# Kernel tuning notes

Measured on AMD Instinct MI355X. Metric: run time of the kernel, lower is better.

## Reference

```python
import jax, jax.numpy as jnp
import numpy as np

N = 100000   # nodes
E = 1600000  # edges
IN = 32      # in_channels
ED = 16      # edge_dim
G = 128      # num graphs in batch
NEG = 0.01   # LeakyReLU default slope

def lrelu(v):
    return jnp.where(v > 0, v, NEG * v)

def gine_conv(x, src, dst, edge_attr, We, be, Wa, ba, Wb, bb):
    # PyG GINEConv (eps=0): out = nn(x + sum_{j->i} relu(x_j + lin(edge_attr)))
    e = edge_attr @ We + be                      # [E, d]
    m = jax.nn.relu(x[src] + e)                  # gather + add + relu
    agg = jax.ops.segment_sum(m, dst, num_segments=x.shape[0])
    h = x + agg
    return lrelu(h @ Wa + ba) @ Wb + bb

def setup_inputs() -> dict:
    key = jax.random.key(0)
    ks = jax.random.split(key, 24)
    w = lambda k, shape: (jax.random.normal(k, shape, dtype=jnp.float32) * 0.05)
    inp = {
        "x": jax.random.normal(ks[0], (N, IN), dtype=jnp.float32),
        "edge_index": jax.random.randint(ks[1], (2, E), 0, N),
        "edge_attr": jax.random.normal(ks[2], (E, ED), dtype=jnp.float32),
        "batch": jnp.sort(jax.random.randint(ks[3], (N,), 0, G)),
        # conv1: edge lin ED->IN, nn IN->32->64
        "We1": w(ks[4], (ED, IN)), "be1": w(ks[5], (IN,)),
        "W1a": w(ks[6], (IN, 32)), "b1a": w(ks[7], (32,)),
        "W1b": w(ks[8], (32, 64)), "b1b": w(ks[9], (64,)),
        # conv2: edge lin ED->64, nn 64->128->256
        "We2": w(ks[10], (ED, 64)), "be2": w(ks[11], (64,)),
        "W2a": w(ks[12], (64, 128)), "b2a": w(ks[13], (128,)),
        "W2b": w(ks[14], (128, 256)), "b2b": w(ks[15], (256,)),
        # head
        "Wf0": w(ks[16], (256, 128)), "bf0": w(ks[17], (128,)),
        "Wf1": w(ks[18], (128, 64)), "bf1": w(ks[19], (64,)),
        "Wf2": w(ks[20], (64, 32)), "bf2": w(ks[21], (32,)),
        "Wr": w(ks[22], (32, 1)), "br": w(ks[23], (1,)),
    }
    return inp

def reference(x, edge_index, edge_attr, batch,
              We1, be1, W1a, b1a, W1b, b1b,
              We2, be2, W2a, b2a, W2b, b2b,
              Wf0, bf0, Wf1, bf1, Wf2, bf2, Wr, br):
    src, dst = edge_index[0], edge_index[1]
    h = gine_conv(x, src, dst, edge_attr, We1, be1, W1a, b1a, W1b, b1b)
    h = lrelu(h)
    h = gine_conv(h, src, dst, edge_attr, We2, be2, W2a, b2a, W2b, b2b)
    h = lrelu(h)
    # global_add_pool over graph ids
    g = jax.ops.segment_sum(h, batch, num_segments=G)   # [G, 256]
    g = lrelu(g @ Wf0 + bf0)
    # dropout: identity (inference reference)
    g = lrelu(g @ Wf1 + bf1)
    g = lrelu(g @ Wf2 + bf2)
    out = (g @ Wr + br)[:, 0]                           # squeeze(dim=1)
    return out
```

## Files before the change

### kernel.cpp

```cpp
#include <hip/hip_runtime.h>

__device__ __forceinline__ float lrelu(float v){ return v > 0.f ? v : 0.01f*v; }

typedef __attribute__((ext_vector_type(8))) short v8s;
typedef __attribute__((ext_vector_type(4))) float v4f;

__device__ __forceinline__ unsigned short f2bf(float f){
    union{float f; unsigned int i;} v; v.f = f;
    unsigned int u = v.i;
    return (unsigned short)((u + 0x7fffu + ((u >> 16) & 1u)) >> 16);
}
__device__ __forceinline__ unsigned int pack2(float a, float b){
    return (unsigned int)f2bf(a) | ((unsigned int)f2bf(b) << 16);
}
__device__ __forceinline__ float bflo(unsigned int u){
    union{unsigned int i; float f;} v; v.i = u << 16; return v.f;
}
__device__ __forceinline__ float bfhi(unsigned int u){
    union{unsigned int i; float f;} v; v.i = u & 0xffff0000u; return v.f;
}
__device__ __forceinline__ float bf2f(unsigned short s){
    union{unsigned int i; float f;} v; v.i = ((unsigned int)s) << 16; return v.f;
}

__global__ __launch_bounds__(256) void k_hist(
    const int* __restrict__ ei, int* __restrict__ deg, int E)
{
    int e = blockIdx.x * 256 + threadIdx.x;
    if (e >= E) return;
    atomicAdd(&deg[ei[E + e]], 1);
}

__global__ __launch_bounds__(256) void k_scan1(
    const int* __restrict__ deg, int* __restrict__ rowptr,
    int* __restrict__ bsum, int N)
{
    __shared__ int sh[256];
    int t = threadIdx.x;
    int i = blockIdx.x * 256 + t;
    int v = (i < N) ? deg[i] : 0;
    sh[t] = v;
    __syncthreads();
    #pragma unroll
    for (int off = 1; off < 256; off <<= 1) {
        int add = (t >= off) ? sh[t - off] : 0;
        __syncthreads();
        sh[t] += add;
        __syncthreads();
    }
    if (i < N) rowptr[i] = sh[t] - v;
    if (t == 255) bsum[blockIdx.x] = sh[t];
}

__global__ __launch_bounds__(512) void k_scan2(int* __restrict__ bsum, int nb)
{
    __shared__ int sh[512];
    int t = threadIdx.x;
    int v = (t < nb) ? bsum[t] : 0;
    sh[t] = v;
    __syncthreads();
    #pragma unroll
    for (int off = 1; off < 512; off <<= 1) {
        int add = (t >= off) ? sh[t - off] : 0;
        __syncthreads();
        sh[t] += add;
        __syncthreads();
    }
    if (t < nb) bsum[t] = sh[t] - v;
}

__global__ __launch_bounds__(256) void k_scan3(
    int* __restrict__ rowptr, int* __restrict__ cursor,
    const int* __restrict__ bsum, int N)
{
    int i = blockIdx.x * 256 + threadIdx.x;
    if (i >= N) return;
    int rp = rowptr[i] + bsum[i >> 8];
    rowptr[i] = rp;
    cursor[i] = rp;
}

__global__ __launch_bounds__(256) void k_castx(
    const float* __restrict__ x, unsigned int* __restrict__ xb, int M8)
{
    int i = blockIdx.x * 256 + threadIdx.x;
    if (i >= M8) return;
    const float4* p = reinterpret_cast<const float4*>(x) + (size_t)i * 2;
    float4 a = p[0], b = p[1];
    uint4 o;
    o.x = pack2(a.x, a.y); o.y = pack2(a.z, a.w);
    o.z = pack2(b.x, b.y); o.w = pack2(b.z, b.w);
    reinterpret_cast<uint4*>(xb)[i] = o;
}

__global__ __launch_bounds__(256) void k_castw(
    const float* __restrict__ W2a, const float* __restrict__ W2b,
    const float* __restrict__ We1, const float* __restrict__ We2,
    unsigned short* __restrict__ W2aT, unsigned short* __restrict__ W2bT,
    unsigned short* __restrict__ WeT1, unsigned short* __restrict__ WeT2)
{
    int i = blockIdx.x * 256 + threadIdx.x;
    if (i < 128 * 64) {
        int n = i >> 6, k = i & 63;
        W2aT[i] = f2bf(W2a[k * 128 + n]);
    }
    int j = i - 128 * 64;
    if (j >= 0 && j < 256 * 128) {
        int n = j >> 7, k = j & 127;
        W2bT[j] = f2bf(W2b[k * 256 + n]);
    }
    int q1 = i - (128 * 64 + 256 * 128);
    if (q1 >= 0 && q1 < 32 * 32) {
        int cch = q1 >> 5, k = q1 & 31;
        WeT1[q1] = (k < 16) ? f2bf(We1[k * 32 + cch]) : (unsigned short)0;
    }
    int q2 = q1 - 32 * 32;
    if (q2 >= 0 && q2 < 64 * 32) {
        int cch = q2 >> 5, k = q2 & 31;
        WeT2[q2] = (k < 16) ? f2bf(We2[k * 64 + cch]) : (unsigned short)0;
    }
}

#define RCHUNK 2048
__global__ __launch_bounds__(256) void k_scatter(
    const int* __restrict__ ei, const float* __restrict__ ea,
    int* __restrict__ cursor, int2* __restrict__ csr2,
    uint4* __restrict__ eab, int E, int N)
{
    const int r = blockIdx.x & 7;
    const int c = blockIdx.x >> 3;
    const int rspan = (N + 7) >> 3;
    const int lo = r * rspan;
    const int hi = lo + rspan;
    int base = c * RCHUNK;
    int end = base + RCHUNK; if (end > E) end = E;
    for (int e = base + threadIdx.x; e < end; e += 256) {
        int d = ei[E + e];
        if (d >= lo && d < hi) {
            int s = ei[e];
            int slot = atomicAdd(&cursor[d], 1);
            const float4* p = reinterpret_cast<const float4*>(ea) + (size_t)e * 4;
            float4 a = p[0], b = p[1], cc = p[2], f = p[3];
            uint4 o0, o1;
            o0.x = pack2(a.x, a.y);  o0.y = pack2(a.z, a.w);
            o0.z = pack2(b.x, b.y);  o0.w = pack2(b.z, b.w);
            o1.x = pack2(cc.x, cc.y); o1.y = pack2(cc.z, cc.w);
            o1.z = pack2(f.x, f.y);  o1.w = pack2(f.z, f.w);
            eab[(size_t)slot * 2]     = o0;
            eab[(size_t)slot * 2 + 1] = o1;
            int2 rr; rr.x = s; rr.y = d;
            csr2[slot] = rr;
        }
    }
}

#define AGG_SPW 64

__global__ __launch_bounds__(256) void k_agg2(
    const unsigned short* __restrict__ xb,
    const uint4* __restrict__ eab,
    const unsigned short* __restrict__ WeT,
    const float* __restrict__ be,
    const int2* __restrict__ csr2, float* __restrict__ agg, int E)
{
    __shared__ __align__(16) float lds[4][2][16][68];
    const int tid  = threadIdx.x;
    const int wv   = tid >> 6;
    const int lane = tid & 63;
    const int lid  = lane & 15;
    const int quad = lane >> 4;
    const int wave = __builtin_amdgcn_readfirstlane((blockIdx.x * 256 + tid) >> 6);
    const int s0 = wave * AGG_SPW;
    if (s0 >= E) return;
    const int nsl = (s0 + AGG_SPW <= E) ? AGG_SPW : E - s0;

    v8s af0 = *reinterpret_cast<const v8s*>(WeT + lid * 32 + quad * 8);
    v8s af1 = *reinterpret_cast<const v8s*>(WeT + (16 + lid) * 32 + quad * 8);
    v8s af2 = *reinterpret_cast<const v8s*>(WeT + (32 + lid) * 32 + quad * 8);
    v8s af3 = *reinterpret_cast<const v8s*>(WeT + (48 + lid) * 32 + quad * 8);
    const float biasc = be[lane];
    const int2*  cp = csr2 + s0;
    const uint4* ep = eab + (size_t)s0 * 2;

    unsigned short xv[2][16];
    int dsv[2][16];
    float acc = 0.f;
    int   cur = cp[0].y;
    bool  owned = false;

    auto GATHER = [&](int t) {
        const int base = t * 16;
        const int cnt = nsl - base;
        #pragma unroll
        for (int e = 0; e < 16; ++e) {
            int ee = (e < cnt) ? e : cnt - 1;
            int2 r = cp[base + ee];
            dsv[t & 1][e] = r.y;
            xv[t & 1][e] = xb[(unsigned)r.x * 64u + (unsigned)lane];
        }
    };
    auto MFMA = [&](int t) {
        int sl = t * 16 + lid;
        if (sl > nsl - 1) sl = nsl - 1;
        uint4 bw = {0u, 0u, 0u, 0u};
        if (quad < 2) bw = ep[2 * sl + quad];
        union { uint4 u; v8s s; } uu; uu.u = bw;
        v8s bf = uu.s;
        v4f d0 = {0.f, 0.f, 0.f, 0.f}, d1 = d0, d2 = d0, d3 = d0;
        d0 = __builtin_amdgcn_mfma_f32_16x16x32_bf16(af0, bf, d0, 0, 0, 0);
        d1 = __builtin_amdgcn_mfma_f32_16x16x32_bf16(af1, bf, d1, 0, 0, 0);
        d2 = __builtin_amdgcn_mfma_f32_16x16x32_bf16(af2, bf, d2, 0, 0, 0);
        d3 = __builtin_amdgcn_mfma_f32_16x16x32_bf16(af3, bf, d3, 0, 0, 0);
        float* lp = &lds[wv][t & 1][lid][quad * 4];
        *reinterpret_cast<v4f*>(lp)      = d0;
        *reinterpret_cast<v4f*>(lp + 16) = d1;
        *reinterpret_cast<v4f*>(lp + 32) = d2;
        *reinterpret_cast<v4f*>(lp + 48) = d3;
    };
    auto ACCUM = [&](int t) {
        const int cnt = nsl - t * 16;
        #pragma unroll
        for (int e = 0; e < 16; ++e) {
            if (e < cnt) {
                float ls = lds[wv][t & 1][e][lane];
                float m = ls + biasc + bf2f(xv[t & 1][e]);
                m = m > 0.f ? m : 0.f;
                int d = dsv[t & 1][e];
                if (d != cur) {
                    if (owned) agg[(unsigned)cur * 64u + lane] = acc;
                    else       atomicAdd(&agg[(unsigned)cur * 64u + lane], acc);
                    acc = 0.f; cur = d; owned = true;
                }
                acc += m;
            }
        }
    };

    GATHER(0); MFMA(0);
    #pragma unroll
    for (int t = 0; t < 4; ++t) {
        if (t * 16 < nsl) {
            if ((t + 1) < 4 && (t + 1) * 16 < nsl) { GATHER(t + 1); MFMA(t + 1); }
            ACCUM(t);
        }
    }
    atomicAdd(&agg[(unsigned)cur * 64u + lane], acc);
}

__global__ __launch_bounds__(256) void k_agg1(
    const unsigned short* __restrict__ xb,
    const uint4* __restrict__ eab,
    const unsigned short* __restrict__ WeT,
    const float* __restrict__ be,
    const int2* __restrict__ csr2, float* __restrict__ agg, int E)
{
    __shared__ __align__(16) float lds[4][2][16][36];
    const int tid  = threadIdx.x;
    const int wv   = tid >> 6;
    const int lane = tid & 63;
    const int lid  = lane & 15;
    const int quad = lane >> 4;
    const int c    = lane & 31;
    const int sub  = lane >> 5;
    const int wave = __builtin_amdgcn_readfirstlane((blockIdx.x * 256 + tid) >> 6);
    const int s0 = wave * AGG_SPW;
    if (s0 >= E) return;
    const int nsl = (s0 + AGG_SPW <= E) ? AGG_SPW : E - s0;

    v8s af0 = *reinterpret_cast<const v8s*>(WeT + lid * 32 + quad * 8);
    v8s af1 = *reinterpret_cast<const v8s*>(WeT + (16 + lid) * 32 + quad * 8);
    const float biasc = be[c];
    const int2*  cp = csr2 + s0;
    const uint4* ep = eab + (size_t)s0 * 2;

    unsigned short xv[2][8];
    int dsv[2][8];
    float acc = 0.f;
    int cur = cp[(sub < nsl) ? sub : 0].y;

    auto GATHER = [&](int t) {
        #pragma unroll
        for (int i = 0; i < 8; ++i) {
            int e = t * 16 + 2 * i + sub;
            int ee = (e < nsl) ? e : nsl - 1;
            int2 r = cp[ee];
            dsv[t & 1][i] = r.y;
            xv[t & 1][i] = xb[(unsigned)r.x * 32u + (unsigned)c];
        }
    };
    auto MFMA = [&](int t) {
        int sl = t * 16 + lid;
        if (sl > nsl - 1) sl = nsl - 1;
        uint4 bw = {0u, 0u, 0u, 0u};
        if (quad < 2) bw = ep[2 * sl + quad];
        union { uint4 u; v8s s; } uu; uu.u = bw;
        v8s bf = uu.s;
        v4f d0 = {0.f, 0.f, 0.f, 0.f}, d1 = d0;
        d0 = __builtin_amdgcn_mfma_f32_16x16x32_bf16(af0, bf, d0, 0, 0, 0);
        d1 = __builtin_amdgcn_mfma_f32_16x16x32_bf16(af1, bf, d1, 0, 0, 0);
        float* lp = &lds[wv][t & 1][lid][quad * 4];
        *reinterpret_cast<v4f*>(lp)      = d0;
        *reinterpret_cast<v4f*>(lp + 16) = d1;
    };
    auto ACCUM = [&](int t) {
        #pragma unroll
        for (int i = 0; i < 8; ++i) {
            int e = t * 16 + 2 * i + sub;
            if (e < nsl) {
                float ls = lds[wv][t & 1][2 * i + sub][c];
                float m = ls + biasc + bf2f(xv[t & 1][i]);
                m = m > 0.f ? m : 0.f;
                int d = dsv[t & 1][i];
                if (d != cur) {
                    atomicAdd(&agg[(unsigned)cur * 32u + c], acc);
                    acc = 0.f; cur = d;
                }
                acc += m;
            }
        }
    };

    GATHER(0); MFMA(0);
    #pragma unroll
    for (int t = 0; t < 4; ++t) {
        if (t * 16 < nsl) {
            if ((t + 1) < 4 && (t + 1) * 16 < nsl) { GATHER(t + 1); MFMA(t + 1); }
            ACCUM(t);
        }
    }
    atomicAdd(&agg[(unsigned)cur * 32u + c], acc);
}

__global__ __launch_bounds__(256, 4) void k_mlp1(
    const float* __restrict__ x, const float* __restrict__ agg1,
    const float* __restrict__ W1a, const float* __restrict__ b1a,
    const float* __restrict__ W1b, const float* __restrict__ b1b,
    unsigned int* __restrict__ h1b, int N)
{
    __shared__ float ts[64][33];
    const int tid = threadIdx.x;
    const int n0 = blockIdx.x * 64;
    const int row = tid & 63;
    const int grp = __builtin_amdgcn_readfirstlane(tid >> 6);
    const int g = n0 + row;

    float hv[32];
    if (g < N) {
        const float4* xp = reinterpret_cast<const float4*>(x) + (size_t)g * 8;
        const float4* ap = reinterpret_cast<const float4*>(agg1) + (size_t)g * 8;
        #pragma unroll
        for (int q = 0; q < 8; ++q) {
            float4 a = xp[q], b = ap[q];
            hv[4*q+0]=a.x+b.x; hv[4*q+1]=a.y+b.y;
            hv[4*q+2]=a.z+b.z; hv[4*q+3]=a.w+b.w;
        }
    } else {
        #pragma unroll
        for (int q = 0; q < 32; ++q) hv[q] = 0.f;
    }

    {
        const int c0 = grp * 8;
        float acc[8];
        #pragma unroll
        for (int i = 0; i < 8; ++i) acc[i] = b1a[c0 + i];
        for (int k = 0; k < 32; ++k) {
            float h = hv[k];
            const float* w = W1a + k*32 + c0;
            #pragma unroll
            for (int i = 0; i < 8; ++i) acc[i] = fmaf(h, w[i], acc[i]);
        }
        #pragma unroll
        for (int i = 0; i < 8; ++i) ts[row][c0 + i] = lrelu(acc[i]);
    }
    __syncthreads();

    {
        const int c0 = grp * 16;
        float acc[16];
        #pragma unroll
        for (int i = 0; i < 16; ++i) acc[i] = b1b[c0 + i];
        for (int k = 0; k < 32; ++k) {
            float tv = ts[row][k];
            const float* w = W1b + k*64 + c0;
            #pragma unroll
            for (int i = 0; i < 16; ++i) acc[i] = fmaf(tv, w[i], acc[i]);
        }
        if (g < N) {
            #pragma unroll
            for (int i = 0; i < 16; ++i) acc[i] = lrelu(acc[i]);
            uint4 p0, p1;
            p0.x = pack2(acc[0],  acc[1]);  p0.y = pack2(acc[2],  acc[3]);
            p0.z = pack2(acc[4],  acc[5]);  p0.w = pack2(acc[6],  acc[7]);
            p1.x = pack2(acc[8],  acc[9]);  p1.y = pack2(acc[10], acc[11]);
            p1.z = pack2(acc[12], acc[13]); p1.w = pack2(acc[14], acc[15]);
            uint4* bp = reinterpret_cast<uint4*>(h1b + (size_t)g*32 + (c0>>1));
            bp[0] = p0; bp[1] = p1;
        }
    }
}

__global__ __launch_bounds__(256) void k_mlp2(
    const unsigned int* __restrict__ h1b, const float* __restrict__ agg2,
    const unsigned short* __restrict__ W2aT, const float* __restrict__ b2a,
    const unsigned short* __restrict__ W2bT, const float* __restrict__ b2b,
    unsigned short* __restrict__ h2b, int N)
{
    __shared__ unsigned short hs[64][72];
    __shared__ unsigned short ts[64][136];
    const int tid = threadIdx.x;
    const int n0 = blockIdx.x * 64;

    {
        int r = tid >> 2, cseg = (tid & 3) * 16;
        int g = n0 + r;
        uint4 o0 = {0,0,0,0}, o1 = {0,0,0,0};
        if (g < N) {
            const uint4* hp = reinterpret_cast<const uint4*>(
                                  h1b + (size_t)g*32 + (cseg>>1));
            const float4* ap = reinterpret_cast<const float4*>(agg2)
                               + (size_t)g*16 + (cseg>>2);
            uint4 u0 = hp[0], u1 = hp[1];
            float4 b0=ap[0], b1=ap[1], b2=ap[2], b3=ap[3];
            o0.x = pack2(bflo(u0.x)+b0.x, bfhi(u0.x)+b0.y);
            o0.y = pack2(bflo(u0.y)+b0.z, bfhi(u0.y)+b0.w);
            o0.z = pack2(bflo(u0.z)+b1.x, bfhi(u0.z)+b1.y);
            o0.w = pack2(bflo(u0.w)+b1.z, bfhi(u0.w)+b1.w);
            o1.x = pack2(bflo(u1.x)+b2.x, bfhi(u1.x)+b2.y);
            o1.y = pack2(bflo(u1.y)+b2.z, bfhi(u1.y)+b2.w);
            o1.z = pack2(bflo(u1.z)+b3.x, bfhi(u1.z)+b3.y);
            o1.w = pack2(bflo(u1.w)+b3.z, bfhi(u1.w)+b3.w);
        }
        uint4* dp = reinterpret_cast<uint4*>(&hs[r][cseg]);
        dp[0] = o0; dp[1] = o1;
    }
    __syncthreads();

    const int wv   = __builtin_amdgcn_readfirstlane(tid >> 6);
    const int lane = tid & 63;
    const int lid  = lane & 15;
    const int quad = lane >> 4;

    v8s afA0 = *reinterpret_cast<const v8s*>(&hs[wv*16 + lid][quad*8]);
    v8s afA1 = *reinterpret_cast<const v8s*>(&hs[wv*16 + lid][32 + quad*8]);
    #pragma unroll
    for (int nt = 0; nt < 8; ++nt) {
        v4f acc = {0.f, 0.f, 0.f, 0.f};
        const unsigned short* wp = W2aT + (nt*16 + lid)*64 + quad*8;
        v8s b0 = *reinterpret_cast<const v8s*>(wp);
        v8s b1 = *reinterpret_cast<const v8s*>(wp + 32);
        acc = __builtin_amdgcn_mfma_f32_16x16x32_bf16(afA0, b0, acc, 0, 0, 0);
        acc = __builtin_amdgcn_mfma_f32_16x16x32_bf16(afA1, b1, acc, 0, 0, 0);
        float bias = b2a[nt*16 + lid];
        #pragma unroll
        for (int i = 0; i < 4; ++i) {
            float v = lrelu(acc[i] + bias);
            ts[wv*16 + quad*4 + i][nt*16 + lid] = f2bf(v);
        }
    }
    __syncthreads();

    v8s afB[4];
    #pragma unroll
    for (int ks = 0; ks < 4; ++ks)
        afB[ks] = *reinterpret_cast<const v8s*>(&ts[wv*16 + lid][ks*32 + quad*8]);
    const int gbase = n0 + wv*16 + quad*4;
    #pragma unroll 4
    for (int nt = 0; nt < 16; ++nt) {
        v4f acc = {0.f, 0.f, 0.f, 0.f};
        const unsigned short* wp = W2bT + (nt*16 + lid)*128 + quad*8;
        #pragma unroll
        for (int ks = 0; ks < 4; ++ks) {
            v8s bf = *reinterpret_cast<const v8s*>(wp + ks*32);
            acc = __builtin_amdgcn_mfma_f32_16x16x32_bf16(afB[ks], bf, acc, 0, 0, 0);
        }
        float bias = b2b[nt*16 + lid];
        #pragma unroll
        for (int i = 0; i < 4; ++i) {
            int g = gbase + i;
            if (g < N) {
                float v = lrelu(acc[i] + bias);
                h2b[(size_t)g*256 + nt*16 + lid] = f2bf(v);
            }
        }
    }
}

__global__ __launch_bounds__(256) void k_pool(
    const unsigned int* __restrict__ h2b, const int* __restrict__ batch,
    float* __restrict__ g, int N)
{
    int tid = threadIdx.x;
    int c2 = tid & 127;
    int h = tid >> 7;
    int base = blockIdx.x * 128;
    int n0 = base + h;
    int nend = base + 128; if (nend > N) nend = N;
    if (n0 >= N) return;
    float acc0 = 0.f, acc1 = 0.f;
    int cur = batch[n0];
    for (int n = n0; n < nend; n += 2) {
        int b = batch[n];
        unsigned int hv = h2b[(size_t)n * 128 + c2];
        if (b != cur) {
            atomicAdd(&g[(unsigned)cur * 256 + 2*c2],     acc0);
            atomicAdd(&g[(unsigned)cur * 256 + 2*c2 + 1], acc1);
            acc0 = acc1 = 0.f; cur = b;
        }
        acc0 += bflo(hv); acc1 += bfhi(hv);
    }
    atomicAdd(&g[(unsigned)cur * 256 + 2*c2],     acc0);
    atomicAdd(&g[(unsigned)cur * 256 + 2*c2 + 1], acc1);
}

__global__ __launch_bounds__(256) void k_head(
    const float* __restrict__ g,
    const float* __restrict__ Wf0, const float* __restrict__ bf0,
    const float* __restrict__ Wf1, const float* __restrict__ bf1,
    const float* __restrict__ Wf2, const float* __restrict__ bf2,
    const float* __restrict__ Wr,  const float* __restrict__ br,
    float* __restrict__ out)
{
    __shared__ float buf[256];
    __shared__ float t0[128];
    __shared__ float t1[64];
    __shared__ float t2[32];
    int gid = blockIdx.x, tid = threadIdx.x;
    buf[tid] = g[(size_t)gid*256 + tid];
    __syncthreads();
    if (tid < 128) {
        float acc = bf0[tid];
        for (int k = 0; k < 256; ++k) acc = fmaf(buf[k], Wf0[k*128 + tid], acc);
        t0[tid] = lrelu(acc);
    }
    __syncthreads();
    if (tid < 64) {
        float acc = bf1[tid];
        for (int k = 0; k < 128; ++k) acc = fmaf(t0[k], Wf1[k*64 + tid], acc);
        t1[tid] = lrelu(acc);
    }
    __syncthreads();
    if (tid < 32) {
        float acc = bf2[tid];
        for (int k = 0; k < 64; ++k) acc = fmaf(t1[k], Wf2[k*32 + tid], acc);
        t2[tid] = lrelu(acc);
    }
    __syncthreads();
    if (tid == 0) {
        float acc = br[0];
        for (int k = 0; k < 32; ++k) acc = fmaf(t2[k], Wr[k], acc);
        out[gid] = acc;
    }
}

extern "C" void kernel_launch(void* const* d_in, const int* in_sizes, int n_in,
                              void* d_out, int out_size, void* d_ws, size_t ws_size,
                              hipStream_t stream)
{
    const float* x     = (const float*)d_in[0];
    const int*   ei    = (const int*)d_in[1];
    const float* ea    = (const float*)d_in[2];
    const int*   batch = (const int*)d_in[3];
    const float* We1=(const float*)d_in[4],  *be1=(const float*)d_in[5];
    const float* W1a=(const float*)d_in[6],  *b1a=(const float*)d_in[7];
    const float* W1b=(const float*)d_in[8],  *b1b=(const float*)d_in[9];
    const float* We2=(const float*)d_in[10], *be2=(const float*)d_in[11];
    const float* W2a=(const float*)d_in[12], *b2a=(const float*)d_in[13];
    const float* W2b=(const float*)d_in[14], *b2b=(const float*)d_in[15];
    const float* Wf0=(const float*)d_in[16], *bf0=(const float*)d_in[17];
    const float* Wf1=(const float*)d_in[18], *bf1=(const float*)d_in[19];
    const float* Wf2=(const float*)d_in[20], *bf2=(const float*)d_in[21];
    const float* Wr =(const float*)d_in[22], *br =(const float*)d_in[23];

    const int N = in_sizes[0] / 32;
    const int E = in_sizes[1] / 2;
    const int G = out_size;
    const int nb = (N + 255) / 256;
    const int nb64 = (N + 63) / 64;

    char* p = (char*)d_ws;
    int*   deg     = (int*)p;                 p += (size_t)N * 4;
    float* gbuf    = (float*)p;               p += (size_t)G * 256 * 4;
    float* agg1    = (float*)p;               p += (size_t)N * 32 * 4;
    float* agg2    = (float*)p;               p += (size_t)N * 64 * 4;
    size_t zero_bytes = (size_t)(p - (char*)d_ws);
    int*   rowptr  = (int*)p;                 p += (size_t)N * 4;
    int*   cursor  = (int*)p;                 p += (size_t)N * 4;
    int*   bsum    = (int*)p;                 p += 512 * 4;
    p = (char*)(((uintptr_t)p + 63) & ~(uintptr_t)63);
    int2*  csr2    = (int2*)p;                p += (size_t)E * 8;
    uint4* eab     = (uint4*)p;               p += (size_t)E * 32;
    unsigned short* xb   = (unsigned short*)p; p += (size_t)N * 32 * 2;
    unsigned int*   h1b  = (unsigned int*)p;  p += (size_t)N * 64 * 2;
    unsigned short* W2aT = (unsigned short*)p; p += 128 * 64 * 2;
    unsigned short* W2bT = (unsigned short*)p; p += 256 * 128 * 2;
    unsigned short* WeT1 = (unsigned short*)p; p += 32 * 32 * 2;
    unsigned short* WeT2 = (unsigned short*)p; p += 64 * 32 * 2;
    unsigned short* h2b  = (unsigned short*)p; p += (size_t)N * 256 * 2;

    hipMemsetAsync(d_ws, 0, zero_bytes, stream);

    int eb = (E + 255) / 256;

    k_hist   <<<eb, 256, 0, stream>>>(ei, deg, E);
    k_scan1  <<<nb, 256, 0, stream>>>(deg, rowptr, bsum, N);
    k_scan2  <<<1, 512, 0, stream>>>(bsum, nb);
    k_scan3  <<<nb, 256, 0, stream>>>(rowptr, cursor, bsum, N);
    {
        int M8 = N * 32 / 8;
        k_castx<<<(M8 + 255) / 256, 256, 0, stream>>>(x, (unsigned int*)xb, M8);
    }
    {
        int tot = 128*64 + 256*128 + 32*32 + 64*32;
        k_castw<<<(tot + 255) / 256, 256, 0, stream>>>(W2a, W2b, We1, We2,
                                                       W2aT, W2bT, WeT1, WeT2);
    }
    {
        int nchunks = (E + RCHUNK - 1) / RCHUNK;
        k_scatter<<<nchunks * 8, 256, 0, stream>>>(ei, ea, cursor, csr2, eab,
                                                   E, N);
    }

    {
        int waves = (E + AGG_SPW - 1) / AGG_SPW;
        int blocks = (waves + 3) / 4;
        k_agg1<<<blocks, 256, 0, stream>>>(xb, eab, WeT1, be1, csr2, agg1, E);
    }
    k_mlp1<<<nb64, 256, 0, stream>>>(x, agg1, W1a, b1a, W1b, b1b,
                                     (unsigned int*)h1b, N);

    {
        int waves = (E + AGG_SPW - 1) / AGG_SPW;
        int blocks = (waves + 3) / 4;
        k_agg2<<<blocks, 256, 0, stream>>>((const unsigned short*)h1b, eab, WeT2,
                                           be2, csr2, agg2, E);
    }
    k_mlp2<<<nb64, 256, 0, stream>>>(h1b, agg2, W2aT, b2a, W2bT, b2b, h2b, N);

    k_pool<<<(N + 127) / 128, 256, 0, stream>>>((const unsigned int*)h2b, batch,
                                                gbuf, N);
    k_head<<<G, 256, 0, stream>>>(gbuf, Wf0, bf0, Wf1, bf1, Wf2, bf2, Wr, br,
                                  (float*)d_out);
}
```

Baseline: 678.7 us.

## Replace CSR scatter with two-pass bucketed radix-style edge ordering

```diff
diff --git a/kernel.cpp b/kernel.cpp
--- a/kernel.cpp
+++ b/kernel.cpp
@@ -78,6 +78,14 @@
     int rp = rowptr[i] + bsum[i >> 8];
     rowptr[i] = rp;
     cursor[i] = rp;
+}
+
+__global__ __launch_bounds__(512) void k_binit(
+    const int* __restrict__ rowptr, int* __restrict__ bcur, int N)
+{
+    int b = threadIdx.x;
+    int node = b << 8;
+    if (node < N) bcur[b] = rowptr[node];
 }
 
 __global__ __launch_bounds__(256) void k_castx(
@@ -121,36 +129,63 @@
     }
 }
 
-#define RCHUNK 2048
-__global__ __launch_bounds__(256) void k_scatter(
+#define BCH 4096
+__global__ __launch_bounds__(256) void k_bucket(
     const int* __restrict__ ei, const float* __restrict__ ea,
-    int* __restrict__ cursor, int2* __restrict__ csr2,
-    uint4* __restrict__ eab, int E, int N)
-{
-    const int r = blockIdx.x & 7;
-    const int c = blockIdx.x >> 3;
-    const int rspan = (N + 7) >> 3;
-    const int lo = r * rspan;
-    const int hi = lo + rspan;
-    int base = c * RCHUNK;
-    int end = base + RCHUNK; if (end > E) end = E;
-    for (int e = base + threadIdx.x; e < end; e += 256) {
+    int* __restrict__ bcur, int2* __restrict__ sA, uint4* __restrict__ sB,
+    int E)
+{
+    __shared__ int hist[512];
+    __shared__ int base[512];
+    __shared__ int lcur[512];
+    const int tid = threadIdx.x;
+    const int c0 = blockIdx.x * BCH;
+    int cend = c0 + BCH; if (cend > E) cend = E;
+    hist[tid] = 0; hist[tid + 256] = 0;
+    __syncthreads();
+    for (int e = c0 + tid; e < cend; e += 256)
+        atomicAdd(&hist[ei[E + e] >> 8], 1);
+    __syncthreads();
+    {
+        int h0 = hist[tid], h1 = hist[tid + 256];
+        base[tid]       = h0 ? atomicAdd(&bcur[tid], h0) : 0;
+        base[tid + 256] = h1 ? atomicAdd(&bcur[tid + 256], h1) : 0;
+        lcur[tid] = 0; lcur[tid + 256] = 0;
+    }
+    __syncthreads();
+    for (int e = c0 + tid; e < cend; e += 256) {
         int d = ei[E + e];
-        if (d >= lo && d < hi) {
-            int s = ei[e];
-            int slot = atomicAdd(&cursor[d], 1);
-            const float4* p = reinterpret_cast<const float4*>(ea) + (size_t)e * 4;
-            float4 a = p[0], b = p[1], cc = p[2], f = p[3];
-            uint4 o0, o1;
-            o0.x = pack2(a.x, a.y);  o0.y = pack2(a.z, a.w);
-            o0.z = pack2(b.x, b.y);  o0.w = pack2(b.z, b.w);
-            o1.x = pack2(cc.x, cc.y); o1.y = pack2(cc.z, cc.w);
-            o1.z = pack2(f.x, f.y);  o1.w = pack2(f.z, f.w);
-            eab[(size_t)slot * 2]     = o0;
-            eab[(size_t)slot * 2 + 1] = o1;
-            int2 rr; rr.x = s; rr.y = d;
-            csr2[slot] = rr;
-        }
+        int b = d >> 8;
+        int pos = base[b] + atomicAdd(&lcur[b], 1);
+        int s = ei[e];
+        const float4* p = reinterpret_cast<const float4*>(ea) + (size_t)e * 4;
+        float4 a = p[0], bb = p[1], cc = p[2], f = p[3];
+        uint4 o0, o1;
+        o0.x = pack2(a.x, a.y);   o0.y = pack2(a.z, a.w);
+        o0.z = pack2(bb.x, bb.y); o0.w = pack2(bb.z, bb.w);
+        o1.x = pack2(cc.x, cc.y); o1.y = pack2(cc.z, cc.w);
+        o1.z = pack2(f.x, f.y);   o1.w = pack2(f.z, f.w);
+        sB[(size_t)pos * 2]     = o0;
+        sB[(size_t)pos * 2 + 1] = o1;
+        int2 rr; rr.x = s; rr.y = d;
+        sA[pos] = rr;
+    }
+}
+
+__global__ __launch_bounds__(256) void k_order(
+    const int2* __restrict__ sA, const uint4* __restrict__ sB,
+    const int* __restrict__ rowptr, int* __restrict__ cursor,
+    int2* __restrict__ csr2, uint4* __restrict__ eab, int E, int NBK)
+{
+    int b = blockIdx.x;
+    int s0 = rowptr[b << 8];
+    int e0 = (b + 1 < NBK) ? rowptr[(b + 1) << 8] : E;
+    for (int i = s0 + threadIdx.x; i < e0; i += 256) {
+        int2 r = sA[i];
+        int slot = atomicAdd(&cursor[r.y], 1);
+        csr2[slot] = r;
+        eab[(size_t)slot * 2]     = sB[(size_t)i * 2];
+        eab[(size_t)slot * 2 + 1] = sB[(size_t)i * 2 + 1];
     }
 }
 
@@ -577,6 +612,7 @@
     const int G = out_size;
     const int nb = (N + 255) / 256;
     const int nb64 = (N + 63) / 64;
+    const int NBK = (N + 255) >> 8;
 
     char* p = (char*)d_ws;
     int*   deg     = (int*)p;                 p += (size_t)N * 4;
@@ -587,9 +623,11 @@
     int*   rowptr  = (int*)p;                 p += (size_t)N * 4;
     int*   cursor  = (int*)p;                 p += (size_t)N * 4;
     int*   bsum    = (int*)p;                 p += 512 * 4;
+    int*   bcur    = (int*)p;                 p += 512 * 4;
     p = (char*)(((uintptr_t)p + 63) & ~(uintptr_t)63);
     int2*  csr2    = (int2*)p;                p += (size_t)E * 8;
     uint4* eab     = (uint4*)p;               p += (size_t)E * 32;
+    int2*  sA      = (int2*)p;                p += (size_t)E * 8;
     unsigned short* xb   = (unsigned short*)p; p += (size_t)N * 32 * 2;
     unsigned int*   h1b  = (unsigned int*)p;  p += (size_t)N * 64 * 2;
     unsigned short* W2aT = (unsigned short*)p; p += 128 * 64 * 2;
@@ -597,6 +635,7 @@
     unsigned short* WeT1 = (unsigned short*)p; p += 32 * 32 * 2;
     unsigned short* WeT2 = (unsigned short*)p; p += 64 * 32 * 2;
     unsigned short* h2b  = (unsigned short*)p; p += (size_t)N * 256 * 2;
+    uint4* sB = (uint4*)h2b;
 
     hipMemsetAsync(d_ws, 0, zero_bytes, stream);
 
@@ -606,6 +645,7 @@
     k_scan1  <<<nb, 256, 0, stream>>>(deg, rowptr, bsum, N);
     k_scan2  <<<1, 512, 0, stream>>>(bsum, nb);
     k_scan3  <<<nb, 256, 0, stream>>>(rowptr, cursor, bsum, N);
+    k_binit  <<<1, 512, 0, stream>>>(rowptr, bcur, N);
     {
         int M8 = N * 32 / 8;
         k_castx<<<(M8 + 255) / 256, 256, 0, stream>>>(x, (unsigned int*)xb, M8);
@@ -615,11 +655,8 @@
         k_castw<<<(tot + 255) / 256, 256, 0, stream>>>(W2a, W2b, We1, We2,
                                                        W2aT, W2bT, WeT1, WeT2);
     }
-    {
-        int nchunks = (E + RCHUNK - 1) / RCHUNK;
-        k_scatter<<<nchunks * 8, 256, 0, stream>>>(ei, ea, cursor, csr2, eab,
-                                                   E, N);
-    }
+    k_bucket<<<(E + BCH - 1) / BCH, 256, 0, stream>>>(ei, ea, bcur, sA, sB, E);
+    k_order <<<NBK, 256, 0, stream>>>(sA, sB, rowptr, cursor, csr2, eab, E, NBK);
 
     {
         int waves = (E + AGG_SPW - 1) / AGG_SPW;
```

Result: slower. 703.4 us (+3.6%).
